# Kernel optimization log

Hardware: AMD Instinct MI355X
Metric: run time of the kernel (lower is better)

## Reference

```python
import jax, jax.numpy as jnp
import numpy as np

N_EMBED = 512  # c in the original; scale uses sqrt(c), not head_size


def setup_inputs() -> dict:
    key = jax.random.key(0)
    k1, k2, k3, k4 = jax.random.split(key, 4)
    B, T, C, H = 4, 4096, N_EMBED, 64
    x = jax.random.normal(k1, (B, T, C), dtype=jnp.float32)
    Wk = jax.random.normal(k2, (C, H), dtype=jnp.float32) * (1.0 / np.sqrt(C))
    Wq = jax.random.normal(k3, (C, H), dtype=jnp.float32) * (1.0 / np.sqrt(C))
    Wv = jax.random.normal(k4, (C, H), dtype=jnp.float32) * (1.0 / np.sqrt(C))
    return {"x": x, "Wk": Wk, "Wq": Wq, "Wv": Wv}


def reference(x, Wk, Wq, Wv):
    # x: [B, T, C]; Wk/Wq/Wv: [C, H]
    B, T, C = x.shape
    k = jnp.einsum('btc,ch->bth', x, Wk)
    q = jnp.einsum('btc,ch->bth', x, Wq)
    v = jnp.einsum('btc,ch->bth', x, Wv)
    scale = 1.0 / jnp.sqrt(jnp.float32(C))  # original divides by sqrt(c)
    scores = jnp.einsum('bth,bsh->bts', q, k) * scale  # [B, T, T]
    causal = jnp.tril(jnp.ones((T, T), dtype=bool))
    scores = jnp.where(causal, scores, -jnp.inf)
    attn = jax.nn.softmax(scores, axis=-1)
    # dropout = 0.0 -> identity
    out = jnp.einsum('bts,bsh->bth', attn, v)  # [B, T, H]
    return out
```

## Files before the change

### kernel.cpp

```cpp
#include <hip/hip_runtime.h>
#include <hip/hip_bf16.h>
#include <math.h>

#define NB 4
#define NT 4096
#define NC 512
#define NH 64
#define QBLK 64
#define KVBLK 64
#define LDK 72
#define MASKV (-1e30f)

typedef __attribute__((ext_vector_type(8))) short bf16x8;
typedef __attribute__((ext_vector_type(4))) float f32x4;

__device__ inline unsigned short f2bf(float f) {
    __hip_bfloat16 h = __float2bfloat16(f);
    return *reinterpret_cast<unsigned short*>(&h);
}

__device__ inline int part_slot(int b, int qt, int ch) {
    int m = qt >> 3, r = qt & 7;
    return b * 288 + qt + 4 * m * (m - 1) + r * m + ch;
}

__global__ __launch_bounds__(256) void wconv(
    const float* __restrict__ Wk, const float* __restrict__ Wq,
    const float* __restrict__ Wv, unsigned short* __restrict__ Wt)
{
    int idx = blockIdx.x * 256 + threadIdx.x;
    int n = idx % 192, c = idx / 192;
    int sel = n >> 6, h = n & 63;
    const float* W = (sel == 0) ? Wq : (sel == 1) ? Wk : Wv;
    float val = W[c * NH + h];
    if (sel == 0) val *= 0.044194173824159216f;
    Wt[n * NC + c] = f2bf(val);
}

__global__ __launch_bounds__(256) void qkv_gemm(
    const float* __restrict__ x, const unsigned short* __restrict__ Wt,
    unsigned short* __restrict__ q, unsigned short* __restrict__ k,
    unsigned short* __restrict__ v)
{
    __shared__ unsigned short xa[32][LDK];
    __shared__ unsigned short wb[192][LDK];

    const int tid = threadIdx.x;
    const int w = tid >> 6, lane = tid & 63, l15 = lane & 15, g = lane >> 4;
    const size_t r0 = (size_t)blockIdx.x * 32;

    f32x4 acc[2][3];
    #pragma unroll
    for (int mt = 0; mt < 2; ++mt)
        #pragma unroll
        for (int nt = 0; nt < 3; ++nt) acc[mt][nt] = (f32x4){0.f,0.f,0.f,0.f};

    for (int c0 = 0; c0 < NC; c0 += 64) {
        __syncthreads();
        {
            int row = tid >> 3, f8 = tid & 7;
            const float* xp = x + (r0 + row) * NC + c0 + f8*8;
            float4 x0 = *reinterpret_cast<const float4*>(xp);
            float4 x1 = *reinterpret_cast<const float4*>(xp + 4);
            bf16x8 a8;
            a8[0]=f2bf(x0.x); a8[1]=f2bf(x0.y); a8[2]=f2bf(x0.z); a8[3]=f2bf(x0.w);
            a8[4]=f2bf(x1.x); a8[5]=f2bf(x1.y); a8[6]=f2bf(x1.z); a8[7]=f2bf(x1.w);
            *reinterpret_cast<bf16x8*>(&xa[row][f8*8]) = a8;
        }
        #pragma unroll
        for (int i = 0; i < 6; ++i) {
            int idx = tid + 256*i;
            int row = idx >> 3, f8 = idx & 7;
            bf16x8 w8 = *reinterpret_cast<const bf16x8*>(Wt + (size_t)row * NC + c0 + f8*8);
            *reinterpret_cast<bf16x8*>(&wb[row][f8*8]) = w8;
        }
        __syncthreads();

        #pragma unroll
        for (int kk = 0; kk < 2; ++kk) {
            bf16x8 a[2], bfr[3];
            #pragma unroll
            for (int mt = 0; mt < 2; ++mt)
                a[mt] = *reinterpret_cast<const bf16x8*>(&xa[16*mt + l15][32*kk + 8*g]);
            #pragma unroll
            for (int nt = 0; nt < 3; ++nt)
                bfr[nt] = *reinterpret_cast<const bf16x8*>(&wb[48*w + 16*nt + l15][32*kk + 8*g]);
            __builtin_amdgcn_s_setprio(1);
            #pragma unroll
            for (int mt = 0; mt < 2; ++mt)
                #pragma unroll
                for (int nt = 0; nt < 3; ++nt)
                    acc[mt][nt] = __builtin_amdgcn_mfma_f32_16x16x32_bf16(a[mt], bfr[nt], acc[mt][nt], 0, 0, 0);
            __builtin_amdgcn_s_setprio(0);
        }
    }

    #pragma unroll
    for (int mt = 0; mt < 2; ++mt)
        #pragma unroll
        for (int nt = 0; nt < 3; ++nt) {
            int ncol = 48*w + 16*nt + l15;
            int sel = ncol >> 6, h = ncol & 63;
            unsigned short* dst = (sel == 0) ? q : (sel == 1) ? k : v;
            #pragma unroll
            for (int r = 0; r < 4; ++r)
                dst[(r0 + 16*mt + 4*g + r) * NH + h] = f2bf(acc[mt][nt][r]);
        }
}

__global__ __launch_bounds__(256) void attn_part(
    const unsigned short* __restrict__ qg,
    const unsigned short* __restrict__ kg,
    const unsigned short* __restrict__ vg,
    float* __restrict__ out,
    float* __restrict__ O_part,
    float* __restrict__ ML_part)
{
    const int qt = 63 - blockIdx.x;
    const int ch = blockIdx.y;
    if (8*ch > qt) return;
    const int b  = blockIdx.z;
    const int nch = (qt >> 3) + 1;

    __shared__ unsigned short k_lds[2][KVBLK][LDK];
    __shared__ unsigned short vt_lds[2][NH][LDK];
    __shared__ unsigned short p_lds[4][16][LDK];

    const int tid  = threadIdx.x;
    const int w    = tid >> 6;
    const int lane = tid & 63;
    const int l15  = lane & 15;
    const int g    = lane >> 4;

    const int q0 = qt * QBLK;
    const size_t base = (size_t)b * NT * NH;
    const int qrow  = q0 + 16*w + l15;
    const int wrow0 = q0 + 16*w;
    const int qhi   = wrow0 + 15;

    bf16x8 qf0, qf1;
    {
        const unsigned short* qp = qg + base + (size_t)qrow * NH + 8*g;
        qf0 = *reinterpret_cast<const bf16x8*>(qp);
        qf1 = *reinterpret_cast<const bf16x8*>(qp + 32);
    }

    f32x4 ot[4];
    #pragma unroll
    for (int i = 0; i < 4; ++i) ot[i] = (f32x4){0.f,0.f,0.f,0.f};
    float m = MASKV, lsum = 0.f;

    const int tBeg = 8 * ch;
    const int tEnd = min(8 * (ch + 1), qt + 1);

    const int krow = tid >> 3, kc8 = tid & 7;
    const int vd = lane, vkq = w;

    bf16x8 kpre0, kpre1;
    unsigned short vpre[16];

    {
        const int s0 = tBeg * KVBLK;
        const unsigned short* kp = kg + base + (size_t)(s0 + krow) * NH + kc8*8;
        kpre0 = *reinterpret_cast<const bf16x8*>(kp);
        kpre1 = *reinterpret_cast<const bf16x8*>(kp + 32 * NH);
        #pragma unroll
        for (int i = 0; i < 16; ++i)
            vpre[i] = vg[base + (size_t)(s0 + vkq*16 + i) * NH + vd];
    }

    int cur = 0;
    for (int it = tBeg; it < tEnd; ++it) {
        const int s0 = it * KVBLK;
        *reinterpret_cast<bf16x8*>(&k_lds[cur][krow][kc8*8])      = kpre0;
        *reinterpret_cast<bf16x8*>(&k_lds[cur][krow+32][kc8*8])   = kpre1;
        *reinterpret_cast<bf16x8*>(&vt_lds[cur][vd][vkq*16])      = *reinterpret_cast<bf16x8*>(&vpre[0]);
        *reinterpret_cast<bf16x8*>(&vt_lds[cur][vd][vkq*16 + 8])  = *reinterpret_cast<bf16x8*>(&vpre[8]);
        __syncthreads();

        if (it + 1 < tEnd) {
            const int sn = s0 + KVBLK;
            const unsigned short* kp = kg + base + (size_t)(sn + krow) * NH + kc8*8;
            kpre0 = *reinterpret_cast<const bf16x8*>(kp);
            kpre1 = *reinterpret_cast<const bf16x8*>(kp + 32 * NH);
            #pragma unroll
            for (int i = 0; i < 16; ++i)
                vpre[i] = vg[base + (size_t)(sn + vkq*16 + i) * NH + vd];
        }

        if (s0 <= qhi) {
            f32x4 s[4];
            __builtin_amdgcn_s_setprio(1);
            #pragma unroll
            for (int t = 0; t < 4; ++t) {
                bf16x8 ka = *reinterpret_cast<const bf16x8*>(&k_lds[cur][16*t + l15][8*g]);
                bf16x8 kb = *reinterpret_cast<const bf16x8*>(&k_lds[cur][16*t + l15][8*g + 32]);
                s[t] = __builtin_amdgcn_mfma_f32_16x16x32_bf16(ka, qf0, (f32x4){0.f,0.f,0.f,0.f}, 0, 0, 0);
                s[t] = __builtin_amdgcn_mfma_f32_16x16x32_bf16(kb, qf1, s[t], 0, 0, 0);
            }
            __builtin_amdgcn_s_setprio(0);

            if (s0 + 63 > wrow0) {
                const int kvb = s0 + 4*g;
                #pragma unroll
                for (int t = 0; t < 4; ++t)
                    #pragma unroll
                    for (int r = 0; r < 4; ++r)
                        if (kvb + 16*t + r > qrow) s[t][r] = MASKV;
            }

            float pm = MASKV;
            #pragma unroll
            for (int t = 0; t < 4; ++t)
                #pragma unroll
                for (int r = 0; r < 4; ++r) pm = fmaxf(pm, s[t][r]);
            pm = fmaxf(pm, __shfl_xor(pm, 16));
            pm = fmaxf(pm, __shfl_xor(pm, 32));

            if (!__all(pm <= m + 8.f)) {
                float mn   = fmaxf(m, pm);
                float corr = __expf(m - mn);
                lsum *= corr;
                #pragma unroll
                for (int dt = 0; dt < 4; ++dt)
                    #pragma unroll
                    for (int e = 0; e < 4; ++e) ot[dt][e] *= corr;
                m = mn;
            }

            float ps = 0.f;
            #pragma unroll
            for (int t = 0; t < 4; ++t)
                #pragma unroll
                for (int r = 0; r < 4; ++r) {
                    float pv = __expf(s[t][r] - m);
                    s[t][r] = pv;
                    ps += pv;
                }

            #pragma unroll
            for (int t = 0; t < 4; ++t) {
                unsigned int w0 = (unsigned int)f2bf(s[t][0]) | ((unsigned int)f2bf(s[t][1]) << 16);
                unsigned int w1 = (unsigned int)f2bf(s[t][2]) | ((unsigned int)f2bf(s[t][3]) << 16);
                *reinterpret_cast<unsigned int*>(&p_lds[w][l15][16*t + 4*g])     = w0;
                *reinterpret_cast<unsigned int*>(&p_lds[w][l15][16*t + 4*g + 2]) = w1;
            }

            ps += __shfl_xor(ps, 16);
            ps += __shfl_xor(ps, 32);
            lsum += ps;

            __builtin_amdgcn_s_setprio(1);
            #pragma unroll
            for (int kk = 0; kk < 2; ++kk) {
                bf16x8 pf = *reinterpret_cast<const bf16x8*>(&p_lds[w][l15][8*g + 32*kk]);
                #pragma unroll
                for (int dt = 0; dt < 4; ++dt) {
                    bf16x8 vf = *reinterpret_cast<const bf16x8*>(&vt_lds[cur][16*dt + l15][8*g + 32*kk]);
                    ot[dt] = __builtin_amdgcn_mfma_f32_16x16x32_bf16(vf, pf, ot[dt], 0, 0, 0);
                }
            }
            __builtin_amdgcn_s_setprio(0);
        }
        cur ^= 1;
    }

    if (nch == 1) {
        const float inv = 1.f / lsum;
        float* orow = out + base + (size_t)qrow * NH;
        #pragma unroll
        for (int dt = 0; dt < 4; ++dt) {
            f32x4 o4;
            #pragma unroll
            for (int r = 0; r < 4; ++r) o4[r] = ot[dt][r] * inv;
            *reinterpret_cast<f32x4*>(&orow[16*dt + 4*g]) = o4;
        }
    } else {
        const int slot = part_slot(b, qt, ch);
        float* op = O_part + (size_t)slot * (QBLK*NH) + (size_t)(16*w + l15) * NH;
        #pragma unroll
        for (int dt = 0; dt < 4; ++dt)
            *reinterpret_cast<f32x4*>(&op[16*dt + 4*g]) = ot[dt];
        if (g == 0) {
            float2 ml = make_float2(m, lsum);
            *reinterpret_cast<float2*>(&ML_part[(size_t)slot * 128 + 2*(16*w + l15)]) = ml;
        }
    }
}

__global__ __launch_bounds__(256) void attn_merge(
    const float* __restrict__ O_part,
    const float* __restrict__ ML_part,
    float* __restrict__ out)
{
    const int qt = 8 + blockIdx.x;
    const int b  = blockIdx.y;
    const int nch = (qt >> 3) + 1;
    const int slot0 = part_slot(b, qt, 0);
    const int row = threadIdx.x >> 2;
    const int dq  = (threadIdx.x & 3) * 16;

    float M = MASKV;
    #pragma unroll 2
    for (int c = 0; c < nch; ++c)
        M = fmaxf(M, ML_part[(size_t)(slot0 + c) * 128 + 2*row]);

    float L = 0.f;
    float acc[16];
    #pragma unroll
    for (int j = 0; j < 16; ++j) acc[j] = 0.f;

    for (int c = 0; c < nch; ++c) {
        const float* mlp = &ML_part[(size_t)(slot0 + c) * 128 + 2*row];
        float mc = mlp[0], lc = mlp[1];
        float wgt = __expf(mc - M);
        L += wgt * lc;
        const float* op = O_part + (size_t)(slot0 + c) * (QBLK*NH) + (size_t)row * NH + dq;
        #pragma unroll
        for (int j4 = 0; j4 < 4; ++j4) {
            float4 o4 = *reinterpret_cast<const float4*>(op + 4*j4);
            acc[4*j4+0] = fmaf(wgt, o4.x, acc[4*j4+0]);
            acc[4*j4+1] = fmaf(wgt, o4.y, acc[4*j4+1]);
            acc[4*j4+2] = fmaf(wgt, o4.z, acc[4*j4+2]);
            acc[4*j4+3] = fmaf(wgt, o4.w, acc[4*j4+3]);
        }
    }

    const float inv = 1.f / L;
    float* orow = out + (size_t)b * NT * NH + (size_t)(qt * QBLK + row) * NH + dq;
    #pragma unroll
    for (int j4 = 0; j4 < 4; ++j4) {
        float4 o4;
        o4.x = acc[4*j4+0] * inv;
        o4.y = acc[4*j4+1] * inv;
        o4.z = acc[4*j4+2] * inv;
        o4.w = acc[4*j4+3] * inv;
        *reinterpret_cast<float4*>(orow + 4*j4) = o4;
    }
}

extern "C" void kernel_launch(void* const* d_in, const int* in_sizes, int n_in,
                              void* d_out, int out_size, void* d_ws, size_t ws_size,
                              hipStream_t stream) {
    const float* x  = (const float*)d_in[0];
    const float* Wk = (const float*)d_in[1];
    const float* Wq = (const float*)d_in[2];
    const float* Wv = (const float*)d_in[3];
    float* out = (float*)d_out;

    const size_t n = (size_t)NB * NT * NH;
    unsigned short* qb = (unsigned short*)d_ws;
    unsigned short* kb = qb + n;
    unsigned short* vb = kb + n;
    unsigned short* Wt = vb + n;
    float* O_part  = (float*)(Wt + 192 * NC);
    float* ML_part = O_part + (size_t)1152 * QBLK * NH;

    wconv<<<(192*NC)/256, 256, 0, stream>>>(Wk, Wq, Wv, Wt);
    qkv_gemm<<<(NB*NT)/32, 256, 0, stream>>>(x, Wt, qb, kb, vb);

    dim3 pgrid(64, 8, NB);
    attn_part<<<pgrid, 256, 0, stream>>>(qb, kb, vb, out, O_part, ML_part);
    dim3 mgrid(56, NB);
    attn_merge<<<mgrid, 256, 0, stream>>>(O_part, ML_part, out);
}
```

Before: 64.94 us.

## Transpose V in projection, stage full x row in LDS, use exp2 and bf16 partials

The QKV projection now writes V already transposed (head-major), so the attention kernel reads V fragments straight from global memory instead of staging and transposing them through LDS. The projection loads the whole 32x512 x tile into LDS once and streams weight fragments from global memory, dropping the per-chunk weight staging and its barriers. The Q scale now folds in log2(e) so softmax uses exp2f, and split partial outputs are stored as bf16 with a simpler slot layout. Together these cut LDS traffic, barriers and partial-buffer bandwidth, at the cost of more global V and weight loads and lower precision in the merged partials.

```diff
diff --git a/kernel.cpp b/kernel.cpp
--- a/kernel.cpp
+++ b/kernel.cpp
@@ -6,9 +6,9 @@
 #define NT 4096
 #define NC 512
 #define NH 64
-#define QBLK 64
 #define KVBLK 64
 #define LDK 72
+#define LDA 520
 #define MASKV (-1e30f)
 
 typedef __attribute__((ext_vector_type(8))) short bf16x8;
@@ -18,10 +18,9 @@
     __hip_bfloat16 h = __float2bfloat16(f);
     return *reinterpret_cast<unsigned short*>(&h);
 }
-
-__device__ inline int part_slot(int b, int qt, int ch) {
-    int m = qt >> 3, r = qt & 7;
-    return b * 288 + qt + 4 * m * (m - 1) + r * m + ch;
+__device__ inline float bf2f(unsigned int u16bits) {
+    unsigned int u = u16bits << 16;
+    return *reinterpret_cast<float*>(&u);
 }
 
 __global__ __launch_bounds__(256) void wconv(
@@ -33,66 +32,57 @@
     int sel = n >> 6, h = n & 63;
     const float* W = (sel == 0) ? Wq : (sel == 1) ? Wk : Wv;
     float val = W[c * NH + h];
-    if (sel == 0) val *= 0.044194173824159216f;
+    if (sel == 0) val *= 0.063758715f;
     Wt[n * NC + c] = f2bf(val);
 }
 
 __global__ __launch_bounds__(256) void qkv_gemm(
     const float* __restrict__ x, const unsigned short* __restrict__ Wt,
     unsigned short* __restrict__ q, unsigned short* __restrict__ k,
-    unsigned short* __restrict__ v)
+    unsigned short* __restrict__ vt)
 {
-    __shared__ unsigned short xa[32][LDK];
-    __shared__ unsigned short wb[192][LDK];
+    __shared__ unsigned short xa[32][LDA];
 
     const int tid = threadIdx.x;
     const int w = tid >> 6, lane = tid & 63, l15 = lane & 15, g = lane >> 4;
     const size_t r0 = (size_t)blockIdx.x * 32;
 
+    #pragma unroll
+    for (int i = 0; i < 8; ++i) {
+        int idx = tid + 256 * i;
+        int row = idx >> 6, c8 = idx & 63;
+        const float* xp = x + (r0 + row) * NC + c8 * 8;
+        float4 x0 = *reinterpret_cast<const float4*>(xp);
+        float4 x1 = *reinterpret_cast<const float4*>(xp + 4);
+        bf16x8 a8;
+        a8[0]=f2bf(x0.x); a8[1]=f2bf(x0.y); a8[2]=f2bf(x0.z); a8[3]=f2bf(x0.w);
+        a8[4]=f2bf(x1.x); a8[5]=f2bf(x1.y); a8[6]=f2bf(x1.z); a8[7]=f2bf(x1.w);
+        *reinterpret_cast<bf16x8*>(&xa[row][c8 * 8]) = a8;
+    }
+    __syncthreads();
+
     f32x4 acc[2][3];
     #pragma unroll
     for (int mt = 0; mt < 2; ++mt)
         #pragma unroll
         for (int nt = 0; nt < 3; ++nt) acc[mt][nt] = (f32x4){0.f,0.f,0.f,0.f};
 
-    for (int c0 = 0; c0 < NC; c0 += 64) {
-        __syncthreads();
-        {
-            int row = tid >> 3, f8 = tid & 7;
-            const float* xp = x + (r0 + row) * NC + c0 + f8*8;
-            float4 x0 = *reinterpret_cast<const float4*>(xp);
-            float4 x1 = *reinterpret_cast<const float4*>(xp + 4);
-            bf16x8 a8;
-            a8[0]=f2bf(x0.x); a8[1]=f2bf(x0.y); a8[2]=f2bf(x0.z); a8[3]=f2bf(x0.w);
-            a8[4]=f2bf(x1.x); a8[5]=f2bf(x1.y); a8[6]=f2bf(x1.z); a8[7]=f2bf(x1.w);
-            *reinterpret_cast<bf16x8*>(&xa[row][f8*8]) = a8;
-        }
-        #pragma unroll
-        for (int i = 0; i < 6; ++i) {
-            int idx = tid + 256*i;
-            int row = idx >> 3, f8 = idx & 7;
-            bf16x8 w8 = *reinterpret_cast<const bf16x8*>(Wt + (size_t)row * NC + c0 + f8*8);
-            *reinterpret_cast<bf16x8*>(&wb[row][f8*8]) = w8;
-        }
-        __syncthreads();
-
-        #pragma unroll
-        for (int kk = 0; kk < 2; ++kk) {
-            bf16x8 a[2], bfr[3];
-            #pragma unroll
-            for (int mt = 0; mt < 2; ++mt)
-                a[mt] = *reinterpret_cast<const bf16x8*>(&xa[16*mt + l15][32*kk + 8*g]);
-            #pragma unroll
-            for (int nt = 0; nt < 3; ++nt)
-                bfr[nt] = *reinterpret_cast<const bf16x8*>(&wb[48*w + 16*nt + l15][32*kk + 8*g]);
-            __builtin_amdgcn_s_setprio(1);
-            #pragma unroll
-            for (int mt = 0; mt < 2; ++mt)
-                #pragma unroll
-                for (int nt = 0; nt < 3; ++nt)
-                    acc[mt][nt] = __builtin_amdgcn_mfma_f32_16x16x32_bf16(a[mt], bfr[nt], acc[mt][nt], 0, 0, 0);
-            __builtin_amdgcn_s_setprio(0);
-        }
+    const unsigned short* wbase = Wt + (size_t)(48*w + l15) * NC + 8*g;
+    #pragma unroll 2
+    for (int ko = 0; ko < 16; ++ko) {
+        bf16x8 bfr[3];
+        #pragma unroll
+        for (int nt = 0; nt < 3; ++nt)
+            bfr[nt] = *reinterpret_cast<const bf16x8*>(wbase + nt*16*NC + 32*ko);
+        bf16x8 a0 = *reinterpret_cast<const bf16x8*>(&xa[l15][32*ko + 8*g]);
+        bf16x8 a1 = *reinterpret_cast<const bf16x8*>(&xa[16 + l15][32*ko + 8*g]);
+        __builtin_amdgcn_s_setprio(1);
+        #pragma unroll
+        for (int nt = 0; nt < 3; ++nt) {
+            acc[0][nt] = __builtin_amdgcn_mfma_f32_16x16x32_bf16(a0, bfr[nt], acc[0][nt], 0, 0, 0);
+            acc[1][nt] = __builtin_amdgcn_mfma_f32_16x16x32_bf16(a1, bfr[nt], acc[1][nt], 0, 0, 0);
+        }
+        __builtin_amdgcn_s_setprio(0);
     }
 
     #pragma unroll
@@ -101,29 +91,30 @@
         for (int nt = 0; nt < 3; ++nt) {
             int ncol = 48*w + 16*nt + l15;
             int sel = ncol >> 6, h = ncol & 63;
-            unsigned short* dst = (sel == 0) ? q : (sel == 1) ? k : v;
-            #pragma unroll
-            for (int r = 0; r < 4; ++r)
-                dst[(r0 + 16*mt + 4*g + r) * NH + h] = f2bf(acc[mt][nt][r]);
+            if (sel < 2) {
+                unsigned short* dst = (sel == 0) ? q : k;
+                #pragma unroll
+                for (int r = 0; r < 4; ++r)
+                    dst[(r0 + 16*mt + 4*g + r) * NH + h] = f2bf(acc[mt][nt][r]);
+            } else {
+                int bb = (int)(r0 >> 12);
+                int trow = ((int)r0 & (NT-1)) + 16*mt + 4*g;
+                unsigned int lo = (unsigned int)f2bf(acc[mt][nt][0]) | ((unsigned int)f2bf(acc[mt][nt][1]) << 16);
+                unsigned int hi = (unsigned int)f2bf(acc[mt][nt][2]) | ((unsigned int)f2bf(acc[mt][nt][3]) << 16);
+                *reinterpret_cast<uint2*>(&vt[((size_t)bb*NH + h)*NT + trow]) = make_uint2(lo, hi);
+            }
         }
 }
 
 __global__ __launch_bounds__(256) void attn_part(
     const unsigned short* __restrict__ qg,
     const unsigned short* __restrict__ kg,
-    const unsigned short* __restrict__ vg,
+    const unsigned short* __restrict__ vtg,
     float* __restrict__ out,
-    float* __restrict__ O_part,
+    unsigned short* __restrict__ O_part,
     float* __restrict__ ML_part)
 {
-    const int qt = 63 - blockIdx.x;
-    const int ch = blockIdx.y;
-    if (8*ch > qt) return;
-    const int b  = blockIdx.z;
-    const int nch = (qt >> 3) + 1;
-
     __shared__ unsigned short k_lds[2][KVBLK][LDK];
-    __shared__ unsigned short vt_lds[2][NH][LDK];
     __shared__ unsigned short p_lds[4][16][LDK];
 
     const int tid  = threadIdx.x;
@@ -132,11 +123,15 @@
     const int l15  = lane & 15;
     const int g    = lane >> 4;
 
-    const int q0 = qt * QBLK;
+    const int qt = 63 - blockIdx.x;
+    const int ch = blockIdx.y;
+    if (8 * ch > qt) return;
+    const int b  = blockIdx.z;
+
+    const int q0 = qt * 64;
     const size_t base = (size_t)b * NT * NH;
-    const int qrow  = q0 + 16*w + l15;
-    const int wrow0 = q0 + 16*w;
-    const int qhi   = wrow0 + 15;
+    const int qrow = q0 + 16*w + l15;
+    const int qhi  = q0 + 16*w + 15;
 
     bf16x8 qf0, qf1;
     {
@@ -151,75 +146,81 @@
     float m = MASKV, lsum = 0.f;
 
     const int tBeg = 8 * ch;
-    const int tEnd = min(8 * (ch + 1), qt + 1);
-
-    const int krow = tid >> 3, kc8 = tid & 7;
-    const int vd = lane, vkq = w;
-
+    const int tEnd = min(8 * ch + 8, qt + 1);
+
+    const int srow = tid >> 3, sc8 = tid & 7;
     bf16x8 kpre0, kpre1;
-    unsigned short vpre[16];
 
     {
-        const int s0 = tBeg * KVBLK;
-        const unsigned short* kp = kg + base + (size_t)(s0 + krow) * NH + kc8*8;
-        kpre0 = *reinterpret_cast<const bf16x8*>(kp);
-        kpre1 = *reinterpret_cast<const bf16x8*>(kp + 32 * NH);
-        #pragma unroll
-        for (int i = 0; i < 16; ++i)
-            vpre[i] = vg[base + (size_t)(s0 + vkq*16 + i) * NH + vd];
-    }
-
-    int cur = 0;
-    for (int it = tBeg; it < tEnd; ++it) {
-        const int s0 = it * KVBLK;
-        *reinterpret_cast<bf16x8*>(&k_lds[cur][krow][kc8*8])      = kpre0;
-        *reinterpret_cast<bf16x8*>(&k_lds[cur][krow+32][kc8*8])   = kpre1;
-        *reinterpret_cast<bf16x8*>(&vt_lds[cur][vd][vkq*16])      = *reinterpret_cast<bf16x8*>(&vpre[0]);
-        *reinterpret_cast<bf16x8*>(&vt_lds[cur][vd][vkq*16 + 8])  = *reinterpret_cast<bf16x8*>(&vpre[8]);
+        const unsigned short* kp = kg + base + (size_t)(tBeg*64 + srow) * NH + sc8*8;
+        bf16x8 k0 = *reinterpret_cast<const bf16x8*>(kp);
+        bf16x8 k1 = *reinterpret_cast<const bf16x8*>(kp + 32*NH);
+        *reinterpret_cast<bf16x8*>(&k_lds[0][srow][sc8*8])      = k0;
+        *reinterpret_cast<bf16x8*>(&k_lds[0][srow + 32][sc8*8]) = k1;
+        if (tBeg + 1 < tEnd) {
+            const unsigned short* kp2 = kg + base + (size_t)((tBeg+1)*64 + srow) * NH + sc8*8;
+            kpre0 = *reinterpret_cast<const bf16x8*>(kp2);
+            kpre1 = *reinterpret_cast<const bf16x8*>(kp2 + 32*NH);
+        }
         __syncthreads();
-
-        if (it + 1 < tEnd) {
-            const int sn = s0 + KVBLK;
-            const unsigned short* kp = kg + base + (size_t)(sn + krow) * NH + kc8*8;
-            kpre0 = *reinterpret_cast<const bf16x8*>(kp);
-            kpre1 = *reinterpret_cast<const bf16x8*>(kp + 32 * NH);
-            #pragma unroll
-            for (int i = 0; i < 16; ++i)
-                vpre[i] = vg[base + (size_t)(sn + vkq*16 + i) * NH + vd];
-        }
-
-        if (s0 <= qhi) {
-            f32x4 s[4];
+    }
+
+    for (int t = tBeg; t < tEnd; ++t) {
+        const int cur = (t - tBeg) & 1;
+        const int s0  = t * 64;
+        const bool active = (s0 <= qhi);
+
+        f32x4 s[4];
+        if (active) {
             __builtin_amdgcn_s_setprio(1);
             #pragma unroll
-            for (int t = 0; t < 4; ++t) {
-                bf16x8 ka = *reinterpret_cast<const bf16x8*>(&k_lds[cur][16*t + l15][8*g]);
-                bf16x8 kb = *reinterpret_cast<const bf16x8*>(&k_lds[cur][16*t + l15][8*g + 32]);
-                s[t] = __builtin_amdgcn_mfma_f32_16x16x32_bf16(ka, qf0, (f32x4){0.f,0.f,0.f,0.f}, 0, 0, 0);
-                s[t] = __builtin_amdgcn_mfma_f32_16x16x32_bf16(kb, qf1, s[t], 0, 0, 0);
+            for (int t4 = 0; t4 < 4; ++t4) {
+                bf16x8 ka = *reinterpret_cast<const bf16x8*>(&k_lds[cur][16*t4 + l15][8*g]);
+                bf16x8 kb = *reinterpret_cast<const bf16x8*>(&k_lds[cur][16*t4 + l15][8*g + 32]);
+                s[t4] = __builtin_amdgcn_mfma_f32_16x16x32_bf16(ka, qf0, (f32x4){0.f,0.f,0.f,0.f}, 0, 0, 0);
+                s[t4] = __builtin_amdgcn_mfma_f32_16x16x32_bf16(kb, qf1, s[t4], 0, 0, 0);
             }
             __builtin_amdgcn_s_setprio(0);
-
-            if (s0 + 63 > wrow0) {
-                const int kvb = s0 + 4*g;
-                #pragma unroll
-                for (int t = 0; t < 4; ++t)
+        }
+
+        if (t + 1 < tEnd) {
+            *reinterpret_cast<bf16x8*>(&k_lds[cur^1][srow][sc8*8])      = kpre0;
+            *reinterpret_cast<bf16x8*>(&k_lds[cur^1][srow + 32][sc8*8]) = kpre1;
+            if (t + 2 < tEnd) {
+                const unsigned short* kp = kg + base + (size_t)((t+2)*64 + srow) * NH + sc8*8;
+                kpre0 = *reinterpret_cast<const bf16x8*>(kp);
+                kpre1 = *reinterpret_cast<const bf16x8*>(kp + 32*NH);
+            }
+        }
+
+        if (active) {
+            const unsigned short* vbase = vtg + ((size_t)b*NH + l15)*NT + s0 + 8*g;
+            bf16x8 vf[4][2];
+            #pragma unroll
+            for (int dt = 0; dt < 4; ++dt)
+                #pragma unroll
+                for (int kk = 0; kk < 2; ++kk)
+                    vf[dt][kk] = *reinterpret_cast<const bf16x8*>(vbase + (size_t)dt*16*NT + kk*32);
+
+            if (s0 + 63 > q0 + 16*w) {
+                #pragma unroll
+                for (int t4 = 0; t4 < 4; ++t4)
                     #pragma unroll
                     for (int r = 0; r < 4; ++r)
-                        if (kvb + 16*t + r > qrow) s[t][r] = MASKV;
+                        if (s0 + 16*t4 + 4*g + r > qrow) s[t4][r] = MASKV;
             }
 
             float pm = MASKV;
             #pragma unroll
-            for (int t = 0; t < 4; ++t)
-                #pragma unroll
-                for (int r = 0; r < 4; ++r) pm = fmaxf(pm, s[t][r]);
+            for (int t4 = 0; t4 < 4; ++t4)
+                #pragma unroll
+                for (int r = 0; r < 4; ++r) pm = fmaxf(pm, s[t4][r]);
             pm = fmaxf(pm, __shfl_xor(pm, 16));
             pm = fmaxf(pm, __shfl_xor(pm, 32));
 
             if (!__all(pm <= m + 8.f)) {
-                float mn   = fmaxf(m, pm);
-                float corr = __expf(m - mn);
+                float mn = fmaxf(m, pm);
+                float corr = exp2f(m - mn);
                 lsum *= corr;
                 #pragma unroll
                 for (int dt = 0; dt < 4; ++dt)
@@ -230,42 +231,42 @@
 
             float ps = 0.f;
             #pragma unroll
-            for (int t = 0; t < 4; ++t)
+            for (int t4 = 0; t4 < 4; ++t4)
                 #pragma unroll
                 for (int r = 0; r < 4; ++r) {
-                    float pv = __expf(s[t][r] - m);
-                    s[t][r] = pv;
+                    float pv = exp2f(s[t4][r] - m);
+                    s[t4][r] = pv;
                     ps += pv;
                 }
 
             #pragma unroll
-            for (int t = 0; t < 4; ++t) {
-                unsigned int w0 = (unsigned int)f2bf(s[t][0]) | ((unsigned int)f2bf(s[t][1]) << 16);
-                unsigned int w1 = (unsigned int)f2bf(s[t][2]) | ((unsigned int)f2bf(s[t][3]) << 16);
-                *reinterpret_cast<unsigned int*>(&p_lds[w][l15][16*t + 4*g])     = w0;
-                *reinterpret_cast<unsigned int*>(&p_lds[w][l15][16*t + 4*g + 2]) = w1;
+            for (int t4 = 0; t4 < 4; ++t4) {
+                unsigned int w0 = (unsigned int)f2bf(s[t4][0]) | ((unsigned int)f2bf(s[t4][1]) << 16);
+                unsigned int w1 = (unsigned int)f2bf(s[t4][2]) | ((unsigned int)f2bf(s[t4][3]) << 16);
+                *reinterpret_cast<unsigned int*>(&p_lds[w][l15][16*t4 + 4*g])     = w0;
+                *reinterpret_cast<unsigned int*>(&p_lds[w][l15][16*t4 + 4*g + 2]) = w1;
             }
 
             ps += __shfl_xor(ps, 16);
             ps += __shfl_xor(ps, 32);
             lsum += ps;
 
+            bf16x8 pf[2];
+            pf[0] = *reinterpret_cast<const bf16x8*>(&p_lds[w][l15][8*g]);
+            pf[1] = *reinterpret_cast<const bf16x8*>(&p_lds[w][l15][8*g + 32]);
             __builtin_amdgcn_s_setprio(1);
             #pragma unroll
-            for (int kk = 0; kk < 2; ++kk) {
-                bf16x8 pf = *reinterpret_cast<const bf16x8*>(&p_lds[w][l15][8*g + 32*kk]);
-                #pragma unroll
-                for (int dt = 0; dt < 4; ++dt) {
-                    bf16x8 vf = *reinterpret_cast<const bf16x8*>(&vt_lds[cur][16*dt + l15][8*g + 32*kk]);
-                    ot[dt] = __builtin_amdgcn_mfma_f32_16x16x32_bf16(vf, pf, ot[dt], 0, 0, 0);
-                }
-            }
+            for (int kk = 0; kk < 2; ++kk)
+                #pragma unroll
+                for (int dt = 0; dt < 4; ++dt)
+                    ot[dt] = __builtin_amdgcn_mfma_f32_16x16x32_bf16(vf[dt][kk], pf[kk], ot[dt], 0, 0, 0);
             __builtin_amdgcn_s_setprio(0);
         }
-        cur ^= 1;
-    }
-
-    if (nch == 1) {
+
+        __syncthreads();
+    }
+
+    if (qt < 8) {
         const float inv = 1.f / lsum;
         float* orow = out + base + (size_t)qrow * NH;
         #pragma unroll
@@ -276,32 +277,34 @@
             *reinterpret_cast<f32x4*>(&orow[16*dt + 4*g]) = o4;
         }
     } else {
-        const int slot = part_slot(b, qt, ch);
-        float* op = O_part + (size_t)slot * (QBLK*NH) + (size_t)(16*w + l15) * NH;
-        #pragma unroll
-        for (int dt = 0; dt < 4; ++dt)
-            *reinterpret_cast<f32x4*>(&op[16*dt + 4*g]) = ot[dt];
+        const int slot = (b*64 + qt)*8 + ch;
+        unsigned short* op = O_part + (size_t)slot * 4096 + (size_t)(16*w + l15) * NH;
+        #pragma unroll
+        for (int dt = 0; dt < 4; ++dt) {
+            unsigned int lo = (unsigned int)f2bf(ot[dt][0]) | ((unsigned int)f2bf(ot[dt][1]) << 16);
+            unsigned int hi = (unsigned int)f2bf(ot[dt][2]) | ((unsigned int)f2bf(ot[dt][3]) << 16);
+            *reinterpret_cast<uint2*>(&op[16*dt + 4*g]) = make_uint2(lo, hi);
+        }
         if (g == 0) {
-            float2 ml = make_float2(m, lsum);
-            *reinterpret_cast<float2*>(&ML_part[(size_t)slot * 128 + 2*(16*w + l15)]) = ml;
+            *reinterpret_cast<float2*>(&ML_part[(size_t)slot * 128 + 2*(16*w + l15)]) =
+                make_float2(m, lsum);
         }
     }
 }
 
 __global__ __launch_bounds__(256) void attn_merge(
-    const float* __restrict__ O_part,
+    const unsigned short* __restrict__ O_part,
     const float* __restrict__ ML_part,
     float* __restrict__ out)
 {
     const int qt = 8 + blockIdx.x;
     const int b  = blockIdx.y;
     const int nch = (qt >> 3) + 1;
-    const int slot0 = part_slot(b, qt, 0);
+    const int slot0 = (b*64 + qt)*8;
     const int row = threadIdx.x >> 2;
     const int dq  = (threadIdx.x & 3) * 16;
 
     float M = MASKV;
-    #pragma unroll 2
     for (int c = 0; c < nch; ++c)
         M = fmaxf(M, ML_part[(size_t)(slot0 + c) * 128 + 2*row]);
 
@@ -312,22 +315,25 @@
 
     for (int c = 0; c < nch; ++c) {
         const float* mlp = &ML_part[(size_t)(slot0 + c) * 128 + 2*row];
-        float mc = mlp[0], lc = mlp[1];
-        float wgt = __expf(mc - M);
-        L += wgt * lc;
-        const float* op = O_part + (size_t)(slot0 + c) * (QBLK*NH) + (size_t)row * NH + dq;
-        #pragma unroll
-        for (int j4 = 0; j4 < 4; ++j4) {
-            float4 o4 = *reinterpret_cast<const float4*>(op + 4*j4);
-            acc[4*j4+0] = fmaf(wgt, o4.x, acc[4*j4+0]);
-            acc[4*j4+1] = fmaf(wgt, o4.y, acc[4*j4+1]);
-            acc[4*j4+2] = fmaf(wgt, o4.z, acc[4*j4+2]);
-            acc[4*j4+3] = fmaf(wgt, o4.w, acc[4*j4+3]);
+        float wgt = exp2f(mlp[0] - M);
+        L += wgt * mlp[1];
+        const unsigned short* op = O_part + (size_t)(slot0 + c) * 4096 + (size_t)row * NH + dq;
+        #pragma unroll
+        for (int h = 0; h < 2; ++h) {
+            uint4 pk = *reinterpret_cast<const uint4*>(op + 8*h);
+            acc[8*h+0] = fmaf(wgt, bf2f(pk.x & 0xffff), acc[8*h+0]);
+            acc[8*h+1] = fmaf(wgt, bf2f(pk.x >> 16),    acc[8*h+1]);
+            acc[8*h+2] = fmaf(wgt, bf2f(pk.y & 0xffff), acc[8*h+2]);
+            acc[8*h+3] = fmaf(wgt, bf2f(pk.y >> 16),    acc[8*h+3]);
+            acc[8*h+4] = fmaf(wgt, bf2f(pk.z & 0xffff), acc[8*h+4]);
+            acc[8*h+5] = fmaf(wgt, bf2f(pk.z >> 16),    acc[8*h+5]);
+            acc[8*h+6] = fmaf(wgt, bf2f(pk.w & 0xffff), acc[8*h+6]);
+            acc[8*h+7] = fmaf(wgt, bf2f(pk.w >> 16),    acc[8*h+7]);
         }
     }
 
     const float inv = 1.f / L;
-    float* orow = out + (size_t)b * NT * NH + (size_t)(qt * QBLK + row) * NH + dq;
+    float* orow = out + (size_t)b * NT * NH + (size_t)(qt * 64 + row) * NH + dq;
     #pragma unroll
     for (int j4 = 0; j4 < 4; ++j4) {
         float4 o4;
@@ -351,16 +357,16 @@
     const size_t n = (size_t)NB * NT * NH;
     unsigned short* qb = (unsigned short*)d_ws;
     unsigned short* kb = qb + n;
-    unsigned short* vb = kb + n;
-    unsigned short* Wt = vb + n;
-    float* O_part  = (float*)(Wt + 192 * NC);
-    float* ML_part = O_part + (size_t)1152 * QBLK * NH;
+    unsigned short* vt = kb + n;
+    unsigned short* Wt = vt + n;
+    unsigned short* O_part = Wt + 192 * NC;
+    float* ML_part = (float*)(O_part + (size_t)2048 * 4096);
 
     wconv<<<(192*NC)/256, 256, 0, stream>>>(Wk, Wq, Wv, Wt);
-    qkv_gemm<<<(NB*NT)/32, 256, 0, stream>>>(x, Wt, qb, kb, vb);
+    qkv_gemm<<<(NB*NT)/32, 256, 0, stream>>>(x, Wt, qb, kb, vt);
 
     dim3 pgrid(64, 8, NB);
-    attn_part<<<pgrid, 256, 0, stream>>>(qb, kb, vb, out, O_part, ML_part);
+    attn_part<<<pgrid, 256, 0, stream>>>(qb, kb, vt, out, O_part, ML_part);
     dim3 mgrid(56, NB);
     attn_merge<<<mgrid, 256, 0, stream>>>(O_part, ML_part, out);
 }
```

After: 86.90 us. +33.8%, slower.
